# Kernel optimization log

Measured on AMD Instinct MI355X. Metric: run time of the kernel, lower is better.

## Reference

```python
import jax, jax.numpy as jnp
import numpy as np

N_NODES = 100000
N_EDGES = 1600000
IN_FEAT = 128
N_HEADS = 8
OUT_FEAT = 16


def setup_inputs() -> dict:
    key = jax.random.key(0)
    k1, k2, k3, k4, k5 = jax.random.split(key, 5)
    x = jax.random.normal(k1, (N_NODES, IN_FEAT), dtype=jnp.float32)
    edge_index = jax.random.randint(k2, (2, N_EDGES), 0, N_NODES)
    # Glorot-uniform params as in init_params
    lim_w = float(np.sqrt(6.0 / (IN_FEAT + N_HEADS * OUT_FEAT)))
    W = jax.random.uniform(k3, (IN_FEAT, N_HEADS * OUT_FEAT), minval=-lim_w, maxval=lim_w, dtype=jnp.float32)
    lim_a = float(np.sqrt(6.0 / (1 + N_HEADS * OUT_FEAT)))
    a_src = jax.random.uniform(k4, (N_HEADS, OUT_FEAT), minval=-lim_a, maxval=lim_a, dtype=jnp.float32)
    a_tgt = jax.random.uniform(k5, (N_HEADS, OUT_FEAT), minval=-lim_a, maxval=lim_a, dtype=jnp.float32)
    bias = jnp.zeros((OUT_FEAT,), dtype=jnp.float32)
    return {"in_nodes_features": x, "edge_index": edge_index, "W": W, "a_src": a_src, "a_tgt": a_tgt, "bias": bias}


def reference(in_nodes_features, edge_index, W, a_src, a_tgt, bias):
    # Single GATLayerImp3 with concat=False, activation=Softmax (GAT, num_of_layers=2).
    # Dropout disabled (eval / dropout=0.0).
    N = in_nodes_features.shape[0]
    H, F = a_src.shape
    proj = (in_nodes_features @ W).reshape(N, H, F)            # [N, H, F]
    s_src = jnp.einsum('nhf,hf->nh', proj, a_src)              # [N, H]
    s_tgt = jnp.einsum('nhf,hf->nh', proj, a_tgt)              # [N, H]
    src, tgt = edge_index[0], edge_index[1]
    # lift + per-edge LeakyReLU(0.2) scoring
    e = jax.nn.leaky_relu(s_src[src] + s_tgt[tgt], negative_slope=0.2)  # [E, H]
    # numerically stable segment softmax over edges sharing a target node
    seg_max = jax.ops.segment_max(e, tgt, num_segments=N)      # [N, H]
    seg_max = jnp.where(jnp.isfinite(seg_max), seg_max, 0.0)
    ex = jnp.exp(e - seg_max[tgt])                             # [E, H]
    denom = jax.ops.segment_sum(ex, tgt, num_segments=N)       # [N, H]
    alpha = ex / (denom[tgt] + 1e-16)                          # [E, H]
    # weighted message + scatter-add aggregation
    msg = proj[src] * alpha[:, :, None]                        # [E, H, F]
    out = jax.ops.segment_sum(msg, tgt, num_segments=N)        # [N, H, F]
    out = out.mean(axis=1) + bias                              # concat=False -> mean over heads
    return jax.nn.softmax(out, axis=-1)                        # final-layer Softmax activation
```

## Files before the change

kernel.cpp:

```cpp
#include <hip/hip_runtime.h>
#include <hip/hip_fp16.h>

#define NN 100000
#define NE 1600000

typedef __attribute__((ext_vector_type(2))) float f32x2;

static __device__ __forceinline__ unsigned short f32_to_bf16_rne(float x) {
    unsigned int u = __float_as_uint(x);
    u += 0x7fff + ((u >> 16) & 1);
    return (unsigned short)(u >> 16);
}
static __device__ __forceinline__ float bf16_to_f32(unsigned int bits16) {
    return __uint_as_float(bits16 << 16);
}

__global__ __launch_bounds__(256) void gemm_score_kernel(const float* __restrict__ x,
                                                         const float* __restrict__ W,
                                                         const float* __restrict__ a_src,
                                                         const float* __restrict__ a_tgt,
                                                         unsigned char* __restrict__ projT8,
                                                         unsigned short* __restrict__ s_src_b,
                                                         unsigned short* __restrict__ s_tgt_b) {
    __shared__ float sXT[32][68];
    __shared__ float sW[32][128];
    const int t = threadIdx.x;
    const int n0 = blockIdx.x * 64;
    const int c0 = (t & 31) * 4;
    const int r0 = t >> 5;
    float acc[8][4];
#pragma unroll
    for (int i = 0; i < 8; i++)
#pragma unroll
        for (int j = 0; j < 4; j++) acc[i][j] = 0.f;

    for (int kt = 0; kt < 128; kt += 32) {
#pragma unroll
        for (int p = 0; p < 2; p++) {
            int idx = t + p * 256;
            int r = idx >> 3;
            int kk = idx & 7;
            float4 v = make_float4(0.f, 0.f, 0.f, 0.f);
            int n = n0 + r;
            if (n < NN) v = *reinterpret_cast<const float4*>(&x[(size_t)n * 128 + kt + kk * 4]);
            sXT[kk * 4 + 0][r] = v.x;
            sXT[kk * 4 + 1][r] = v.y;
            sXT[kk * 4 + 2][r] = v.z;
            sXT[kk * 4 + 3][r] = v.w;
        }
#pragma unroll
        for (int p = 0; p < 4; p++) {
            int idx = t + p * 256;
            int kr = idx >> 5;
            int c4 = idx & 31;
            float4 v = *reinterpret_cast<const float4*>(&W[(size_t)(kt + kr) * 128 + c4 * 4]);
            *reinterpret_cast<float4*>(&sW[kr][c4 * 4]) = v;
        }
        __syncthreads();
#pragma unroll
        for (int k = 0; k < 32; k++) {
            float4 xa = *reinterpret_cast<const float4*>(&sXT[k][r0 * 8]);
            float4 xb = *reinterpret_cast<const float4*>(&sXT[k][r0 * 8 + 4]);
            float4 wv = *reinterpret_cast<const float4*>(&sW[k][c0]);
            float xs[8] = {xa.x, xa.y, xa.z, xa.w, xb.x, xb.y, xb.z, xb.w};
#pragma unroll
            for (int i = 0; i < 8; i++) {
                acc[i][0] += xs[i] * wv.x;
                acc[i][1] += xs[i] * wv.y;
                acc[i][2] += xs[i] * wv.z;
                acc[i][3] += xs[i] * wv.w;
            }
        }
        __syncthreads();
    }
    const int h  = c0 >> 4;
    const int f0 = c0 & 15;
    const float aS0 = a_src[c0], aS1 = a_src[c0 + 1], aS2 = a_src[c0 + 2], aS3 = a_src[c0 + 3];
    const float aT0 = a_tgt[c0], aT1 = a_tgt[c0 + 1], aT2 = a_tgt[c0 + 2], aT3 = a_tgt[c0 + 3];
#pragma unroll
    for (int i = 0; i < 8; i++) {
        int n = n0 + r0 * 8 + i;
        if (n < NN) {
            unsigned char* pT = &projT8[(size_t)n * 128];
            unsigned int e01 = __builtin_amdgcn_cvt_pk_fp8_f32(acc[i][0], acc[i][1], 0, false);
            unsigned int e23 = __builtin_amdgcn_cvt_pk_fp8_f32(acc[i][2], acc[i][3], 0, false);
            pT[(f0 + 0) * 8 + h] = (unsigned char)(e01 & 0xFF);
            pT[(f0 + 1) * 8 + h] = (unsigned char)((e01 >> 8) & 0xFF);
            pT[(f0 + 2) * 8 + h] = (unsigned char)(e23 & 0xFF);
            pT[(f0 + 3) * 8 + h] = (unsigned char)((e23 >> 8) & 0xFF);
            float ss = acc[i][0] * aS0 + acc[i][1] * aS1 + acc[i][2] * aS2 + acc[i][3] * aS3;
            float st = acc[i][0] * aT0 + acc[i][1] * aT1 + acc[i][2] * aT2 + acc[i][3] * aT3;
            ss += __shfl_xor(ss, 1);
            ss += __shfl_xor(ss, 2);
            st += __shfl_xor(st, 1);
            st += __shfl_xor(st, 2);
            if ((t & 3) == 0) {
                s_src_b[(size_t)n * 8 + h] = f32_to_bf16_rne(ss);
                s_tgt_b[(size_t)n * 8 + h] = f32_to_bf16_rne(st);
            }
        }
    }
}

__global__ __launch_bounds__(256) void denom_kernel(const int* __restrict__ src,
                                                    const int* __restrict__ tgt,
                                                    const unsigned short* __restrict__ s_src_b,
                                                    const unsigned short* __restrict__ s_tgt_b,
                                                    __half* __restrict__ denom_h,
                                                    unsigned short* __restrict__ exb) {
    int gid = blockIdx.x * blockDim.x + threadIdx.x;
    int e = gid >> 2;
    if (e >= NE) return;
    int h0 = (gid & 3) * 2;
    int s = src[e], t = tgt[e];
    unsigned int ssp = *reinterpret_cast<const unsigned int*>(&s_src_b[(size_t)s * 8 + h0]);
    unsigned int stp = *reinterpret_cast<const unsigned int*>(&s_tgt_b[(size_t)t * 8 + h0]);
    float v0 = bf16_to_f32(ssp & 0xffffu) + bf16_to_f32(stp & 0xffffu);
    float v1 = bf16_to_f32(ssp >> 16) + bf16_to_f32(stp >> 16);
    v0 = v0 >= 0.f ? v0 : 0.2f * v0;
    v1 = v1 >= 0.f ? v1 : 0.2f * v1;
    float ex0 = expf(v0), ex1 = expf(v1);
    unsigned int pk = (unsigned int)f32_to_bf16_rne(ex0) | ((unsigned int)f32_to_bf16_rne(ex1) << 16);
    *reinterpret_cast<unsigned int*>(&exb[(size_t)e * 8 + h0]) = pk;
    unsafeAtomicAdd(reinterpret_cast<__half2*>(&denom_h[(size_t)t * 8 + h0]),
                    __floats2half2_rn(ex0, ex1));
}

__global__ __launch_bounds__(256) void aggregate_kernel(const int* __restrict__ src,
                                                        const int* __restrict__ tgt,
                                                        const __half* __restrict__ denom_h,
                                                        const unsigned short* __restrict__ exb,
                                                        const unsigned char* __restrict__ projT8,
                                                        __half* __restrict__ out_h) {
    int gid = blockIdx.x * blockDim.x + threadIdx.x;
    int e = gid >> 3;
    if (e >= NE) return;
    int j = gid & 7;
    int s = src[e], t = tgt[e];
    float ex = bf16_to_f32(exb[(size_t)e * 8 + j]);
    float dj = __half2float(denom_h[(size_t)t * 8 + j]);
    float alpha = ex / (dj + 1e-16f);
    uint4 v = *reinterpret_cast<const uint4*>(&projT8[(size_t)s * 128 + j * 16]);
    f32x2 a01 = __builtin_amdgcn_cvt_pk_f32_fp8(v.x, false);
    f32x2 a23 = __builtin_amdgcn_cvt_pk_f32_fp8(v.x, true);
    f32x2 a45 = __builtin_amdgcn_cvt_pk_f32_fp8(v.y, false);
    f32x2 a67 = __builtin_amdgcn_cvt_pk_f32_fp8(v.y, true);
    f32x2 b01 = __builtin_amdgcn_cvt_pk_f32_fp8(v.z, false);
    f32x2 b23 = __builtin_amdgcn_cvt_pk_f32_fp8(v.z, true);
    f32x2 b45 = __builtin_amdgcn_cvt_pk_f32_fp8(v.w, false);
    f32x2 b67 = __builtin_amdgcn_cvt_pk_f32_fp8(v.w, true);
    float pa[8] = {a01.x, a01.y, a23.x, a23.y, a45.x, a45.y, a67.x, a67.y};
    float pb[8] = {b01.x, b01.y, b23.x, b23.y, b45.x, b45.y, b67.x, b67.y};
    float m0 = 0.f, m1 = 0.f;
#pragma unroll
    for (int k = 0; k < 8; k++) {
        float ak = __shfl(alpha, k, 8);
        m0 += ak * pa[k];
        m1 += ak * pb[k];
    }
    unsafeAtomicAdd(reinterpret_cast<__half2*>(&out_h[(size_t)t * 16 + 2 * j]),
                    __floats2half2_rn(m0 * 0.125f, m1 * 0.125f));
}

__global__ __launch_bounds__(256) void softmax_kernel(const __half* __restrict__ out_h,
                                                      const float* __restrict__ bias,
                                                      float* __restrict__ out) {
    int gid = blockIdx.x * blockDim.x + threadIdx.x;
    int n = gid >> 4;
    int lane = gid & 15;
    if (n >= NN) return;
    float v = __half2float(out_h[(size_t)n * 16 + lane]) + bias[lane];
    float mx = v;
#pragma unroll
    for (int m = 1; m < 16; m <<= 1) mx = fmaxf(mx, __shfl_xor(mx, m, 64));
    float ex = expf(v - mx);
    float sum = ex;
#pragma unroll
    for (int m = 1; m < 16; m <<= 1) sum += __shfl_xor(sum, m, 64);
    out[(size_t)n * 16 + lane] = ex / sum;
}

extern "C" void kernel_launch(void* const* d_in, const int* in_sizes, int n_in,
                              void* d_out, int out_size, void* d_ws, size_t ws_size,
                              hipStream_t stream) {
    const float* x     = (const float*)d_in[0];
    const int*   ei    = (const int*)d_in[1];
    const float* W     = (const float*)d_in[2];
    const float* a_src = (const float*)d_in[3];
    const float* a_tgt = (const float*)d_in[4];
    const float* bias  = (const float*)d_in[5];
    float* out = (float*)d_out;

    const int* src = ei;
    const int* tgt = ei + NE;

    char* ws = (char*)d_ws;
    size_t off = 0;
    auto alloc = [&](size_t bytes) {
        char* p = ws + off;
        off += (bytes + 255) & ~(size_t)255;
        return p;
    };
    unsigned char*  projT8  = (unsigned char*)alloc((size_t)NN * 128);
    unsigned short* exb     = (unsigned short*)alloc((size_t)NE * 8 * 2);
    unsigned short* s_src_b = (unsigned short*)alloc((size_t)NN * 8 * 2);
    unsigned short* s_tgt_b = (unsigned short*)alloc((size_t)NN * 8 * 2);
    __half*         denom_h = (__half*)alloc((size_t)NN * 8 * 2);
    __half*         out_h   = (__half*)alloc((size_t)NN * 16 * 2);

    hipMemsetAsync(denom_h, 0, (size_t)NN * 8 * 2, stream);
    hipMemsetAsync(out_h, 0, (size_t)NN * 16 * 2, stream);

    gemm_score_kernel<<<(NN + 63) / 64, 256, 0, stream>>>(x, W, a_src, a_tgt, projT8,
                                                          s_src_b, s_tgt_b);
    denom_kernel<<<((size_t)NE * 4 + 255) / 256, 256, 0, stream>>>(src, tgt, s_src_b, s_tgt_b,
                                                                   denom_h, exb);
    aggregate_kernel<<<((size_t)NE * 8 + 255) / 256, 256, 0, stream>>>(src, tgt, denom_h, exb,
                                                                       projT8, out_h);
    softmax_kernel<<<(NN * 16 + 255) / 256, 256, 0, stream>>>(out_h, bias, out);
}
```

Baseline: 238.4 us.

## Compute node projection GEMM with bf16 MFMA instead of fp32 FMA

Rewrites the projection GEMM to convert x and W to bf16 in shared memory and use 16x16x32 bf16 MFMA instructions, with one wavefront per 16-row tile. The epilogue now writes each node's fp8 projT values as packed 8-byte stores and reduces the attention scores with 16-lane shuffles. This aims to cut the FP32 ALU cost of the GEMM stage and the scattered byte stores. In exchange it loses input precision to bf16, reloads the full W into LDS in every block, and adds more shuffle work in the epilogue.

```diff
diff --git a/kernel.cpp b/kernel.cpp
--- a/kernel.cpp
+++ b/kernel.cpp
@@ -5,6 +5,8 @@
 #define NE 1600000
 
 typedef __attribute__((ext_vector_type(2))) float f32x2;
+typedef __attribute__((ext_vector_type(4))) float f32x4;
+typedef __attribute__((ext_vector_type(8))) short short8x;
 
 static __device__ __forceinline__ unsigned short f32_to_bf16_rne(float x) {
     unsigned int u = __float_as_uint(x);
@@ -22,81 +24,87 @@
                                                          unsigned char* __restrict__ projT8,
                                                          unsigned short* __restrict__ s_src_b,
                                                          unsigned short* __restrict__ s_tgt_b) {
-    __shared__ float sXT[32][68];
-    __shared__ float sW[32][128];
+    __shared__ unsigned short sX[64][136];
+    __shared__ unsigned short sWT[128][136];
     const int t = threadIdx.x;
     const int n0 = blockIdx.x * 64;
-    const int c0 = (t & 31) * 4;
-    const int r0 = t >> 5;
-    float acc[8][4];
-#pragma unroll
-    for (int i = 0; i < 8; i++)
-#pragma unroll
-        for (int j = 0; j < 4; j++) acc[i][j] = 0.f;
-
-    for (int kt = 0; kt < 128; kt += 32) {
-#pragma unroll
-        for (int p = 0; p < 2; p++) {
-            int idx = t + p * 256;
-            int r = idx >> 3;
-            int kk = idx & 7;
-            float4 v = make_float4(0.f, 0.f, 0.f, 0.f);
-            int n = n0 + r;
-            if (n < NN) v = *reinterpret_cast<const float4*>(&x[(size_t)n * 128 + kt + kk * 4]);
-            sXT[kk * 4 + 0][r] = v.x;
-            sXT[kk * 4 + 1][r] = v.y;
-            sXT[kk * 4 + 2][r] = v.z;
-            sXT[kk * 4 + 3][r] = v.w;
+
+#pragma unroll
+    for (int p = 0; p < 8; p++) {
+        int idx = t + p * 256;
+        int r = idx >> 5;
+        int k4 = idx & 31;
+        float4 v = make_float4(0.f, 0.f, 0.f, 0.f);
+        int n = n0 + r;
+        if (n < NN) v = *reinterpret_cast<const float4*>(&x[(size_t)n * 128 + k4 * 4]);
+        ushort4 b;
+        b.x = f32_to_bf16_rne(v.x); b.y = f32_to_bf16_rne(v.y);
+        b.z = f32_to_bf16_rne(v.z); b.w = f32_to_bf16_rne(v.w);
+        *reinterpret_cast<ushort4*>(&sX[r][k4 * 4]) = b;
+    }
+#pragma unroll
+    for (int p = 0; p < 16; p++) {
+        int idx = t + p * 256;
+        int kr = idx >> 5;
+        int c4 = idx & 31;
+        float4 v = *reinterpret_cast<const float4*>(&W[(size_t)kr * 128 + c4 * 4]);
+        sWT[c4 * 4 + 0][kr] = f32_to_bf16_rne(v.x);
+        sWT[c4 * 4 + 1][kr] = f32_to_bf16_rne(v.y);
+        sWT[c4 * 4 + 2][kr] = f32_to_bf16_rne(v.z);
+        sWT[c4 * 4 + 3][kr] = f32_to_bf16_rne(v.w);
+    }
+    __syncthreads();
+
+    const int w = t >> 6;
+    const int l = t & 63;
+    const int f = l & 15;
+    const int kg = l >> 4;
+
+    short8x aF[4];
+#pragma unroll
+    for (int kc = 0; kc < 4; kc++)
+        aF[kc] = *reinterpret_cast<const short8x*>(&sX[w * 16 + f][kc * 32 + kg * 8]);
+
+    f32x4 acc[8];
+#pragma unroll
+    for (int nt = 0; nt < 8; nt++) acc[nt] = (f32x4){0.f, 0.f, 0.f, 0.f};
+
+#pragma unroll
+    for (int kc = 0; kc < 4; kc++) {
+#pragma unroll
+        for (int nt = 0; nt < 8; nt++) {
+            short8x bF = *reinterpret_cast<const short8x*>(&sWT[nt * 16 + f][kc * 32 + kg * 8]);
+            acc[nt] = __builtin_amdgcn_mfma_f32_16x16x32_bf16(aF[kc], bF, acc[nt], 0, 0, 0);
         }
-#pragma unroll
-        for (int p = 0; p < 4; p++) {
-            int idx = t + p * 256;
-            int kr = idx >> 5;
-            int c4 = idx & 31;
-            float4 v = *reinterpret_cast<const float4*>(&W[(size_t)(kt + kr) * 128 + c4 * 4]);
-            *reinterpret_cast<float4*>(&sW[kr][c4 * 4]) = v;
-        }
-        __syncthreads();
-#pragma unroll
-        for (int k = 0; k < 32; k++) {
-            float4 xa = *reinterpret_cast<const float4*>(&sXT[k][r0 * 8]);
-            float4 xb = *reinterpret_cast<const float4*>(&sXT[k][r0 * 8 + 4]);
-            float4 wv = *reinterpret_cast<const float4*>(&sW[k][c0]);
-            float xs[8] = {xa.x, xa.y, xa.z, xa.w, xb.x, xb.y, xb.z, xb.w};
-#pragma unroll
-            for (int i = 0; i < 8; i++) {
-                acc[i][0] += xs[i] * wv.x;
-                acc[i][1] += xs[i] * wv.y;
-                acc[i][2] += xs[i] * wv.z;
-                acc[i][3] += xs[i] * wv.w;
-            }
-        }
-        __syncthreads();
-    }
-    const int h  = c0 >> 4;
-    const int f0 = c0 & 15;
-    const float aS0 = a_src[c0], aS1 = a_src[c0 + 1], aS2 = a_src[c0 + 2], aS3 = a_src[c0 + 3];
-    const float aT0 = a_tgt[c0], aT1 = a_tgt[c0 + 1], aT2 = a_tgt[c0 + 2], aT3 = a_tgt[c0 + 3];
-#pragma unroll
-    for (int i = 0; i < 8; i++) {
-        int n = n0 + r0 * 8 + i;
-        if (n < NN) {
-            unsigned char* pT = &projT8[(size_t)n * 128];
-            unsigned int e01 = __builtin_amdgcn_cvt_pk_fp8_f32(acc[i][0], acc[i][1], 0, false);
-            unsigned int e23 = __builtin_amdgcn_cvt_pk_fp8_f32(acc[i][2], acc[i][3], 0, false);
-            pT[(f0 + 0) * 8 + h] = (unsigned char)(e01 & 0xFF);
-            pT[(f0 + 1) * 8 + h] = (unsigned char)((e01 >> 8) & 0xFF);
-            pT[(f0 + 2) * 8 + h] = (unsigned char)(e23 & 0xFF);
-            pT[(f0 + 3) * 8 + h] = (unsigned char)((e23 >> 8) & 0xFF);
-            float ss = acc[i][0] * aS0 + acc[i][1] * aS1 + acc[i][2] * aS2 + acc[i][3] * aS3;
-            float st = acc[i][0] * aT0 + acc[i][1] * aT1 + acc[i][2] * aT2 + acc[i][3] * aT3;
-            ss += __shfl_xor(ss, 1);
-            ss += __shfl_xor(ss, 2);
-            st += __shfl_xor(st, 1);
-            st += __shfl_xor(st, 2);
-            if ((t & 3) == 0) {
-                s_src_b[(size_t)n * 8 + h] = f32_to_bf16_rne(ss);
-                s_tgt_b[(size_t)n * 8 + h] = f32_to_bf16_rne(st);
+    }
+
+    float aS[8], aT[8];
+#pragma unroll
+    for (int nt = 0; nt < 8; nt++) {
+        aS[nt] = a_src[nt * 16 + f];
+        aT[nt] = a_tgt[nt * 16 + f];
+    }
+#pragma unroll
+    for (int reg = 0; reg < 4; reg++) {
+        int n = n0 + w * 16 + kg * 4 + reg;
+        bool valid = (n < NN);
+        unsigned int p01 = __builtin_amdgcn_cvt_pk_fp8_f32(acc[0][reg], acc[1][reg], 0, false);
+        unsigned int p23 = __builtin_amdgcn_cvt_pk_fp8_f32(acc[2][reg], acc[3][reg], 0, false);
+        unsigned int p45 = __builtin_amdgcn_cvt_pk_fp8_f32(acc[4][reg], acc[5][reg], 0, false);
+        unsigned int p67 = __builtin_amdgcn_cvt_pk_fp8_f32(acc[6][reg], acc[7][reg], 0, false);
+        uint2 st8 = make_uint2((p01 & 0xFFFFu) | (p23 << 16), (p45 & 0xFFFFu) | (p67 << 16));
+        if (valid) *reinterpret_cast<uint2*>(&projT8[(size_t)n * 128 + f * 8]) = st8;
+#pragma unroll
+        for (int nt = 0; nt < 8; nt++) {
+            float psS = acc[nt][reg] * aS[nt];
+            float psT = acc[nt][reg] * aT[nt];
+            psS += __shfl_xor(psS, 1); psS += __shfl_xor(psS, 2);
+            psS += __shfl_xor(psS, 4); psS += __shfl_xor(psS, 8);
+            psT += __shfl_xor(psT, 1); psT += __shfl_xor(psT, 2);
+            psT += __shfl_xor(psT, 4); psT += __shfl_xor(psT, 8);
+            if (valid && f == 0) {
+                s_src_b[(size_t)n * 8 + nt] = f32_to_bf16_rne(psS);
+                s_tgt_b[(size_t)n * 8 + nt] = f32_to_bf16_rne(psT);
             }
         }
     }
```

Result: no change. 239.6 us (+0.5%).
